# Kernel optimization log

Hardware: AMD Instinct MI355X
Metric: run time of the kernel (lower is better)

The kernel has to match this reference:

```python
import jax, jax.numpy as jnp
import numpy as np
import math

B, S, D, H = 2, 1024, 1024, 16
HD = D // H
MAX_ITERS = 4
BETA_0, BETA_DELTA = 0.8, 0.2
MOMENTUM = 0.2
FREQ_FACTOR, PHASE_OFFSET = 2.0, 0.0


def setup_inputs() -> dict:
    key = jax.random.key(0)
    ks = jax.random.split(key, 10)
    s = 1.0 / math.sqrt(D)
    return {
        "x": jax.random.normal(ks[0], (B, S, D), dtype=jnp.float32),
        "Wq": jax.random.normal(ks[1], (D, D), dtype=jnp.float32) * s,
        "bq": jnp.zeros((D,), dtype=jnp.float32),
        "Wk": jax.random.normal(ks[2], (D, D), dtype=jnp.float32) * s,
        "bk": jnp.zeros((D,), dtype=jnp.float32),
        "Wv": jax.random.normal(ks[3], (D, D), dtype=jnp.float32) * s,
        "bv": jnp.zeros((D,), dtype=jnp.float32),
        "Wo": jax.random.normal(ks[4], (D, D), dtype=jnp.float32) * s,
        "bo": jnp.zeros((D,), dtype=jnp.float32),
        "resonance_bias": jnp.zeros((1, H, 1, 1), dtype=jnp.float32),
        "phase_factors": jnp.full((1, H, 1, 1), 0.1, dtype=jnp.float32),
    }


def reference(x, Wq, bq, Wk, bk, Wv, bv, Wo, bo, resonance_bias, phase_factors):
    # Projections -> [B, H, S, HD]
    def split_heads(t):
        return t.reshape(B, S, H, HD).transpose(0, 2, 1, 3)

    q = split_heads(x @ Wq.T + bq)
    k = split_heads(x @ Wk.T + bk)
    v = split_heads(x @ Wv.T + bv)

    scale = 1.0 / math.sqrt(HD)
    attn = None
    for t in range(MAX_ITERS):
        # Phase modulation: shift Q/K by learned per-head phase factors
        t_norm = t / MAX_ITERS
        phase = jnp.sin(jnp.float32(FREQ_FACTOR * t_norm * math.pi + PHASE_OFFSET))
        q_mod = q + phase_factors * phase
        k_mod = k + phase_factors * phase
        # Temperature scheduling: inverse temperature grows each iteration
        beta = BETA_0 + BETA_DELTA * t
        scores = beta * scale * jnp.einsum("bhsd,bhtd->bhst", q_mod, k_mod) + resonance_bias
        attn_new = jax.nn.softmax(scores, axis=-1)
        # Momentum-based attention update
        attn = attn_new if attn is None else MOMENTUM * attn + (1.0 - MOMENTUM) * attn_new

    ctx = jnp.einsum("bhst,bhtd->bhsd", attn, v)  # [B,H,S,HD]
    ctx = ctx.transpose(0, 2, 1, 3).reshape(B, S, D)
    return ctx @ Wo.T + bo
```

## Files before the change

### kernel.cpp

```cpp
#include <hip/hip_runtime.h>
#include <hip/hip_bf16.h>
#include <math.h>

#define BB 2
#define SS 1024
#define DD 1024
#define HH 16
#define HD 64
#define BH (BB*HH)

typedef __attribute__((ext_vector_type(8))) short short8_t;
typedef __attribute__((ext_vector_type(4))) float f32x4;

#if __has_builtin(__builtin_amdgcn_exp2f)
#define EXP2(x) __builtin_amdgcn_exp2f(x)
#else
#define EXP2(x) exp2f(x)
#endif

__device__ __forceinline__ ushort f2bf(float f) {
    union { float f; unsigned u; } a; a.f = f;
    unsigned u = a.u;
    u += 0x7FFFu + ((u >> 16) & 1u);
    return (ushort)(u >> 16);
}
__device__ __forceinline__ float bf2f(ushort b) {
    union { unsigned u; float f; } a; a.u = ((unsigned)b) << 16;
    return a.f;
}
__device__ __forceinline__ unsigned pkbf(float a, float b) {
    unsigned r;
    asm("v_cvt_pk_bf16_f32 %0, %1, %2" : "=v"(r) : "v"(a), "v"(b));
    return r;
}

__global__ __launch_bounds__(256) void cvt_all_kernel(
    const float* __restrict__ x,  const float* __restrict__ wq,
    const float* __restrict__ wk, const float* __restrict__ wv,
    const float* __restrict__ wo,
    ushort* __restrict__ xb,  ushort* __restrict__ wqb, ushort* __restrict__ wkb,
    ushort* __restrict__ wvb, ushort* __restrict__ wob)
{
    int bid = blockIdx.x;
    const float* src; ushort* dst; int off;
    if (bid < 2048) { src = x; dst = xb; off = bid; }
    else {
        int seg = (bid - 2048) >> 10;
        off = (bid - 2048) & 1023;
        if (seg == 0)      { src = wq; dst = wqb; }
        else if (seg == 1) { src = wk; dst = wkb; }
        else if (seg == 2) { src = wv; dst = wvb; }
        else               { src = wo; dst = wob; }
    }
    int i = (off * 256 + threadIdx.x) * 4;
    float4 v = *reinterpret_cast<const float4*>(src + i);
    ushort4 o;
    o.x = f2bf(v.x); o.y = f2bf(v.y); o.z = f2bf(v.z); o.w = f2bf(v.w);
    *reinterpret_cast<ushort4*>(dst + i) = o;
}

template<int BM, int OUT_F32>
__device__ __forceinline__ void gemm_body(
    const ushort* __restrict__ A, const ushort* __restrict__ Bm,
    const float* __restrict__ bias, void* __restrict__ Cout,
    int N, int K, float scale)
{
    constexpr int BK = 32;
    __shared__ ushort lsa[BM * BK];
    __shared__ ushort lsb[128 * BK];
    const int tid  = threadIdx.x;
    const int lane = tid & 63;
    const int wave = tid >> 6;
    constexpr int RI = BM / 32;
    const int wrow = (wave >> 1) * (BM / 2);
    const int wcol = (wave & 1) * 64;
    const int tileM = blockIdx.y * BM;
    const int tileN = blockIdx.x * 128;
    const int fr  = lane & 15;
    const int fks = (lane >> 4) * 8;
    const int l4  = lane >> 2;
    const int lm4 = lane & 3;
    f32x4 acc[RI][4] = {};

    for (int kb = 0; kb < K; kb += BK) {
        __syncthreads();
        #pragma unroll
        for (int i = 0; i < BM / 64; ++i) {
            int chunk = wave * (BM / 64) + i;
            const ushort* g = A + (size_t)(tileM + chunk * 16 + l4) * K + kb + lm4 * 8;
            __builtin_amdgcn_global_load_lds(
                (const __attribute__((address_space(1))) unsigned*)g,
                (__attribute__((address_space(3))) unsigned*)&lsa[chunk * 512], 16, 0, 0);
        }
        #pragma unroll
        for (int i = 0; i < 2; ++i) {
            int chunk = wave * 2 + i;
            const ushort* g = Bm + (size_t)(tileN + chunk * 16 + l4) * K + kb + lm4 * 8;
            __builtin_amdgcn_global_load_lds(
                (const __attribute__((address_space(1))) unsigned*)g,
                (__attribute__((address_space(3))) unsigned*)&lsb[chunk * 512], 16, 0, 0);
        }
        __syncthreads();
        short8_t af[RI], bfg[4];
        #pragma unroll
        for (int r = 0; r < RI; ++r)
            af[r] = *reinterpret_cast<const short8_t*>(&lsa[(wrow + r * 16 + fr) * BK + fks]);
        #pragma unroll
        for (int c = 0; c < 4; ++c)
            bfg[c] = *reinterpret_cast<const short8_t*>(&lsb[(wcol + c * 16 + fr) * BK + fks]);
        #pragma unroll
        for (int r = 0; r < RI; ++r)
            #pragma unroll
            for (int c = 0; c < 4; ++c)
                acc[r][c] = __builtin_amdgcn_mfma_f32_16x16x32_bf16(af[r], bfg[c], acc[r][c], 0, 0, 0);
    }

    const int rr = (lane >> 4) * 4;
    #pragma unroll
    for (int r = 0; r < RI; ++r) {
        #pragma unroll
        for (int c = 0; c < 4; ++c) {
            int n = tileN + wcol + c * 16 + fr;
            float bv = bias[n];
            #pragma unroll
            for (int q = 0; q < 4; ++q) {
                int m = tileM + wrow + r * 16 + rr + q;
                float v = (acc[r][c][q] + bv) * scale;
                if (OUT_F32) ((float*)Cout)[(size_t)m * N + n] = v;
                else         ((ushort*)Cout)[(size_t)m * N + n] = f2bf(v);
            }
        }
    }
}

__global__ __launch_bounds__(256) void gemm_qkv_kernel(
    const ushort* __restrict__ xb,
    const ushort* __restrict__ wq, const ushort* __restrict__ wk, const ushort* __restrict__ wv,
    const float* __restrict__ bq, const float* __restrict__ bk, const float* __restrict__ bv,
    ushort* __restrict__ Qb, ushort* __restrict__ Kb, ushort* __restrict__ Vb, float qscale)
{
    const ushort* Bm; const float* bias; ushort* out; float sc;
    if (blockIdx.z == 0)      { Bm = wq; bias = bq; out = Qb; sc = qscale; }
    else if (blockIdx.z == 1) { Bm = wk; bias = bk; out = Kb; sc = 1.0f; }
    else                      { Bm = wv; bias = bv; out = Vb; sc = 1.0f; }
    gemm_body<128, 0>(xb, Bm, bias, out, DD, DD, sc);
}

__global__ __launch_bounds__(256) void gemm_out_kernel(
    const ushort* __restrict__ ctxb, const ushort* __restrict__ wo,
    const float* __restrict__ bo, float* __restrict__ out)
{
    gemm_body<64, 1>(ctxb, wo, bo, out, DD, DD, 1.0f);
}

__global__ __launch_bounds__(256) void tables_kernel(const ushort* __restrict__ Kb,
                                                     const float* __restrict__ pf,
                                                     float* __restrict__ E1, float* __restrict__ E3,
                                                     ushort* __restrict__ Kh,
                                                     float a1, float a3) {
    int idx = blockIdx.x * blockDim.x + threadIdx.x;
    int j  = idx & (SS - 1);
    int bh = idx >> 10;
    int b = bh >> 4, h = bh & 15;
    const ushort* kr = Kb + (size_t)(b * SS + j) * DD + h * HD;
    ushort* kout = Kh + (size_t)idx * HD;
    float s = 0.f;
    #pragma unroll
    for (int c = 0; c < HD; c += 8) {
        short8_t v = *reinterpret_cast<const short8_t*>(kr + c);
        *reinterpret_cast<short8_t*>(kout + c) = v;
        #pragma unroll
        for (int e = 0; e < 8; ++e) s += bf2f((ushort)v[e]);
    }
    float ph = pf[h];
    E1[idx] = __expf(a1 * ph * s);
    E3[idx] = __expf(a3 * ph * s);
}

__global__ __launch_bounds__(256) void transpose_v_kernel(const ushort* __restrict__ Vb,
                                                          ushort* __restrict__ Vt2) {
    __shared__ ushort t[64][72];
    int bh = blockIdx.x; int b = bh >> 4, h = bh & 15;
    int j0 = blockIdx.y * 64;
    #pragma unroll
    for (int s = 0; s < 2; ++s) {
        int ch = threadIdx.x + s * 256;
        int row = ch >> 3, c = (ch & 7) * 8;
        *reinterpret_cast<short8_t*>(&t[row][c]) =
            *reinterpret_cast<const short8_t*>(Vb + (size_t)(b * SS + j0 + row) * DD + h * HD + c);
    }
    __syncthreads();
    #pragma unroll
    for (int s = 0; s < 2; ++s) {
        int ch = threadIdx.x + s * 256;
        int drow = ch >> 3, c = (ch & 7) * 8;
        short8_t v;
        #pragma unroll
        for (int e = 0; e < 8; ++e) v[e] = (short)t[c + e][drow];
        int kb32 = (j0 + c) >> 5;
        int kk   = c & 31;
        *reinterpret_cast<short8_t*>(
            Vt2 + ((size_t)(bh * (SS / 32) + kb32) * HD + drow) * 32 + kk) = v;
    }
}

__global__ __launch_bounds__(256) void attn_kernel(
    const ushort* __restrict__ Qb, const ushort* __restrict__ Kh,
    const ushort* __restrict__ Vt2, const float* __restrict__ E1,
    const float* __restrict__ E3, ushort* __restrict__ ctxb)
{
    __shared__ ushort ycache[4][32][264];
    __shared__ float lbuf[4][4][32];
    const int wg  = blockIdx.x;
    const int swz = (wg & 7) * 128 + (wg >> 3);
    const int bh  = swz >> 5;
    const int qb  = (swz & 31) * 32;
    const int b = bh >> 4, h = bh & 15;
    const int wave = threadIdx.x >> 6;
    const int lane = threadIdx.x & 63;
    const int fr = lane & 15;
    const int g  = lane >> 4;
    const int fk = g * 8;

    const float wt[4] = {0.008f, 0.032f, 0.16f, 0.8f};

    const ushort* qbase0 = Qb + (size_t)(b * SS + qb + fr) * DD + h * HD;
    const ushort* qbase1 = Qb + (size_t)(b * SS + qb + 16 + fr) * DD + h * HD;
    const short8_t aq0a = *reinterpret_cast<const short8_t*>(qbase0 + fk);
    const short8_t aq1a = *reinterpret_cast<const short8_t*>(qbase0 + 32 + fk);
    const short8_t aq0b = *reinterpret_cast<const short8_t*>(qbase1 + fk);
    const short8_t aq1b = *reinterpret_cast<const short8_t*>(qbase1 + 32 + fk);

    const float* e1h = E1 + bh * SS;
    const float* e3h = E3 + bh * SS;
    const ushort* khead = Kh + (size_t)bh * SS * HD;
    const ushort* vhead = Vt2 + (size_t)bh * (SS / 32) * HD * 32;

    float lA[4][4] = {}, lB[4][4] = {};
    for (int it = 0; it < 4; ++it) {
        const int k0 = wave * 256 + it * 64;
        #pragma unroll
        for (int n = 0; n < 4; ++n) {
            const ushort* kb = khead + (size_t)(k0 + n * 16 + fr) * HD;
            short8_t bk0 = *reinterpret_cast<const short8_t*>(kb + fk);
            short8_t bk1 = *reinterpret_cast<const short8_t*>(kb + 32 + fk);
            f32x4 za = {0.f, 0.f, 0.f, 0.f};
            f32x4 zb = {0.f, 0.f, 0.f, 0.f};
            za = __builtin_amdgcn_mfma_f32_16x16x32_bf16(aq0a, bk0, za, 0, 0, 0);
            za = __builtin_amdgcn_mfma_f32_16x16x32_bf16(aq1a, bk1, za, 0, 0, 0);
            zb = __builtin_amdgcn_mfma_f32_16x16x32_bf16(aq0b, bk0, zb, 0, 0, 0);
            zb = __builtin_amdgcn_mfma_f32_16x16x32_bf16(aq1b, bk1, zb, 0, 0, 0);
            float e1v = e1h[k0 + n * 16 + fr];
            float e3v = e3h[k0 + n * 16 + fr];
            #pragma unroll
            for (int r = 0; r < 4; ++r) {
                float ya  = EXP2(za[r]);
                float ya2 = ya * ya;
                float ya4 = ya2 * ya2;
                float ya6 = ya4 * ya2;
                lA[0][r] += ya4;
                lA[1][r] += ya4 * ya * e1v;
                lA[2][r] += ya6;
                lA[3][r] += ya6 * ya * e3v;
                ycache[wave][g * 4 + r][it * 64 + n * 16 + fr] = f2bf(ya);
                float yb  = EXP2(zb[r]);
                float yb2 = yb * yb;
                float yb4 = yb2 * yb2;
                float yb6 = yb4 * yb2;
                lB[0][r] += yb4;
                lB[1][r] += yb4 * yb * e1v;
                lB[2][r] += yb6;
                lB[3][r] += yb6 * yb * e3v;
                ycache[wave][16 + g * 4 + r][it * 64 + n * 16 + fr] = f2bf(yb);
            }
        }
    }
    #pragma unroll
    for (int t = 0; t < 4; ++t)
        #pragma unroll
        for (int r = 0; r < 4; ++r) {
            float sa = lA[t][r];
            sa += __shfl_xor(sa, 1);
            sa += __shfl_xor(sa, 2);
            sa += __shfl_xor(sa, 4);
            sa += __shfl_xor(sa, 8);
            lA[t][r] = sa;
            float sb = lB[t][r];
            sb += __shfl_xor(sb, 1);
            sb += __shfl_xor(sb, 2);
            sb += __shfl_xor(sb, 4);
            sb += __shfl_xor(sb, 8);
            lB[t][r] = sb;
        }
    if (fr == 0) {
        #pragma unroll
        for (int t = 0; t < 4; ++t)
            #pragma unroll
            for (int r = 0; r < 4; ++r) {
                lbuf[wave][t][g * 4 + r]      = lA[t][r];
                lbuf[wave][t][16 + g * 4 + r] = lB[t][r];
            }
    }
    __syncthreads();

    float wlA[4], wlB[4];
    #pragma unroll
    for (int t = 0; t < 4; ++t) {
        float sa = lbuf[0][t][fr] + lbuf[1][t][fr] + lbuf[2][t][fr] + lbuf[3][t][fr];
        float sb = lbuf[0][t][16 + fr] + lbuf[1][t][16 + fr] + lbuf[2][t][16 + fr] + lbuf[3][t][16 + fr];
        wlA[t] = wt[t] / sa;
        wlB[t] = wt[t] / sb;
    }

    f32x4 caccA[4] = {}, caccB[4] = {};
    union FragU { short8_t s; unsigned u[4]; };
    for (int it = 0; it < 4; ++it) {
        const int k0 = wave * 256 + it * 64;
        #pragma unroll
        for (int half = 0; half < 2; ++half) {
            short8_t ya8 = *reinterpret_cast<const short8_t*>(
                &ycache[wave][fr][it * 64 + half * 32 + fk]);
            short8_t yb8 = *reinterpret_cast<const short8_t*>(
                &ycache[wave][16 + fr][it * 64 + half * 32 + fk]);
            const float* e1p = e1h + k0 + half * 32 + fk;
            const float* e3p = e3h + k0 + half * 32 + fk;
            float4 e1a = *reinterpret_cast<const float4*>(e1p);
            float4 e1b = *reinterpret_cast<const float4*>(e1p + 4);
            float4 e3a = *reinterpret_cast<const float4*>(e3p);
            float4 e3b = *reinterpret_cast<const float4*>(e3p + 4);
            FragU paA, paB;
            #pragma unroll
            for (int i = 0; i < 4; ++i) {
                float pva[2], pvb[2];
                #pragma unroll
                for (int j = 0; j < 2; ++j) {
                    const int e = 2 * i + j;
                    float e1v = (e < 4) ? ((const float*)&e1a)[e] : ((const float*)&e1b)[e - 4];
                    float e3v = (e < 4) ? ((const float*)&e3a)[e] : ((const float*)&e3b)[e - 4];
                    float ya  = bf2f((ushort)ya8[e]);
                    float ya2 = ya * ya;
                    float ya4 = ya2 * ya2;
                    float t1a = fmaf(ya, wlA[1] * e1v, wlA[0]);
                    float t2a = fmaf(ya, wlA[3] * e3v, wlA[2]);
                    pva[j] = ya4 * fmaf(ya2, t2a, t1a);
                    float yb  = bf2f((ushort)yb8[e]);
                    float yb2 = yb * yb;
                    float yb4 = yb2 * yb2;
                    float t1b = fmaf(yb, wlB[1] * e1v, wlB[0]);
                    float t2b = fmaf(yb, wlB[3] * e3v, wlB[2]);
                    pvb[j] = yb4 * fmaf(yb2, t2b, t1b);
                }
                paA.u[i] = pkbf(pva[0], pva[1]);
                paB.u[i] = pkbf(pvb[0], pvb[1]);
            }
            const ushort* vt = vhead + (size_t)((k0 + half * 32) >> 5) * HD * 32;
            #pragma unroll
            for (int n2 = 0; n2 < 4; ++n2) {
                short8_t v = *reinterpret_cast<const short8_t*>(
                    vt + (n2 * 16 + fr) * 32 + fk);
                caccA[n2] = __builtin_amdgcn_mfma_f32_16x16x32_bf16(paA.s, v, caccA[n2], 0, 0, 0);
                caccB[n2] = __builtin_amdgcn_mfma_f32_16x16x32_bf16(paB.s, v, caccB[n2], 0, 0, 0);
            }
        }
    }

    __syncthreads();
    float* ctxp = (float*)&ycache[wave][0][0];
    #pragma unroll
    for (int n2 = 0; n2 < 4; ++n2)
        #pragma unroll
        for (int q = 0; q < 4; ++q) {
            ctxp[(g * 4 + q) * 68 + n2 * 16 + fr]        = caccA[n2][q];
            ctxp[(16 + g * 4 + q) * 68 + n2 * 16 + fr]   = caccB[n2][q];
        }
    __syncthreads();

    const int d0 = (threadIdx.x & 15) * 4;
    float* base = (float*)&ycache[0][0][0];
    #pragma unroll
    for (int rr = 0; rr < 2; ++rr) {
        int row = rr * 16 + (threadIdx.x >> 4);
        float4 s0 = *reinterpret_cast<float4*>(base + 0 * 4224 + row * 68 + d0);
        float4 s1 = *reinterpret_cast<float4*>(base + 1 * 4224 + row * 68 + d0);
        float4 s2 = *reinterpret_cast<float4*>(base + 2 * 4224 + row * 68 + d0);
        float4 s3 = *reinterpret_cast<float4*>(base + 3 * 4224 + row * 68 + d0);
        float ox = s0.x + s1.x + s2.x + s3.x;
        float oy = s0.y + s1.y + s2.y + s3.y;
        float oz = s0.z + s1.z + s2.z + s3.z;
        float ow = s0.w + s1.w + s2.w + s3.w;
        uint2 o;
        o.x = pkbf(ox, oy);
        o.y = pkbf(oz, ow);
        size_t off = (size_t)(b * SS + qb + row) * DD + h * HD + d0;
        *reinterpret_cast<uint2*>(ctxb + off) = o;
    }
}

extern "C" void kernel_launch(void* const* d_in, const int* in_sizes, int n_in,
                              void* d_out, int out_size, void* d_ws, size_t ws_size,
                              hipStream_t stream) {
    const float* x  = (const float*)d_in[0];
    const float* Wq = (const float*)d_in[1];
    const float* bq = (const float*)d_in[2];
    const float* Wk = (const float*)d_in[3];
    const float* bk = (const float*)d_in[4];
    const float* Wv = (const float*)d_in[5];
    const float* bv = (const float*)d_in[6];
    const float* Wo = (const float*)d_in[7];
    const float* bo = (const float*)d_in[8];
    const float* pf = (const float*)d_in[10];

    ushort* xb   = (ushort*)d_ws;
    ushort* wqb  = xb  + (size_t)2 * 1024 * 1024;
    ushort* wkb  = wqb + (size_t)1024 * 1024;
    ushort* wvb  = wkb + (size_t)1024 * 1024;
    ushort* wob  = wvb + (size_t)1024 * 1024;
    ushort* Qb   = wob + (size_t)1024 * 1024;
    ushort* Kb   = Qb  + (size_t)2 * 1024 * 1024;
    ushort* Vb   = Kb  + (size_t)2 * 1024 * 1024;
    ushort* Vt2  = Vb  + (size_t)2 * 1024 * 1024;
    ushort* ctxb = Vt2 + (size_t)2 * 1024 * 1024;
    float*  E1p  = (float*)(ctxb + (size_t)2 * 1024 * 1024);
    float*  E3p  = E1p + (size_t)BH * SS;
    ushort* Kh   = xb;

    float ph[4], ctv[4];
    for (int t = 0; t < 4; ++t) {
        double tn = (double)t / 4.0;
        ph[t]  = sinf((float)(2.0 * tn * M_PI + 0.0));
        ctv[t] = (float)((0.8 + 0.2 * (double)t) * 0.125);
    }
    const double LOG2E = 1.44269504088896340736;
    float qscale = (float)(0.025 * LOG2E);
    float a1 = ctv[1] * ph[1];
    float a3 = ctv[3] * ph[3];

    cvt_all_kernel<<<6144, 256, 0, stream>>>(x, Wq, Wk, Wv, Wo, xb, wqb, wkb, wvb, wob);

    gemm_qkv_kernel<<<dim3(8, 16, 3), 256, 0, stream>>>(xb, wqb, wkb, wvb, bq, bk, bv,
                                                        Qb, Kb, Vb, qscale);

    tables_kernel<<<BH * SS / 256, 256, 0, stream>>>(Kb, pf, E1p, E3p, Kh, a1, a3);
    transpose_v_kernel<<<dim3(BH, SS / 64), 256, 0, stream>>>(Vb, Vt2);

    attn_kernel<<<1024, 256, 0, stream>>>(Qb, Kh, Vt2, E1p, E3p, ctxb);

    gemm_out_kernel<<<dim3(8, 32), 256, 0, stream>>>(ctxb, wob, bo, (float*)d_out);
}
```

Measured before the change: 109.2 us.

## Write K and V in attention layouts from QKV GEMM epilogue, drop transpose kernel

The QKV GEMM epilogue now writes K directly in head-major [bh][j][d] layout and V directly in the blocked transposed layout the attention kernel consumes. This removes the separate V transpose kernel and the K copy inside the tables kernel. The QKV GEMM tile height also drops from 128 to 64, doubling the grid. The scattered 2-byte epilogue stores for V (stride 32 along d) are less coalesced, and smaller tiles reduce operand reuse.

```diff
diff --git a/kernel.cpp b/kernel.cpp
--- a/kernel.cpp
+++ b/kernel.cpp
@@ -63,7 +63,7 @@
 __device__ __forceinline__ void gemm_body(
     const ushort* __restrict__ A, const ushort* __restrict__ Bm,
     const float* __restrict__ bias, void* __restrict__ Cout,
-    int N, int K, float scale)
+    int N, int K, float scale, int omode)
 {
     constexpr int BK = 32;
     __shared__ ushort lsa[BM * BK];
@@ -126,8 +126,19 @@
             for (int q = 0; q < 4; ++q) {
                 int m = tileM + wrow + r * 16 + rr + q;
                 float v = (acc[r][c][q] + bv) * scale;
-                if (OUT_F32) ((float*)Cout)[(size_t)m * N + n] = v;
-                else         ((ushort*)Cout)[(size_t)m * N + n] = f2bf(v);
+                if (OUT_F32) {
+                    ((float*)Cout)[(size_t)m * N + n] = v;
+                } else if (omode == 0) {
+                    ((ushort*)Cout)[(size_t)m * N + n] = f2bf(v);
+                } else {
+                    int bh = ((m >> 10) << 4) + (n >> 6);
+                    int j  = m & 1023;
+                    int d  = n & 63;
+                    if (omode == 2)
+                        ((ushort*)Cout)[((size_t)bh * 1024 + j) * 64 + d] = f2bf(v);
+                    else
+                        ((ushort*)Cout)[(((size_t)(bh * 32 + (j >> 5)) * 64 + d)) * 32 + (j & 31)] = f2bf(v);
+                }
             }
         }
     }
@@ -137,71 +148,40 @@
     const ushort* __restrict__ xb,
     const ushort* __restrict__ wq, const ushort* __restrict__ wk, const ushort* __restrict__ wv,
     const float* __restrict__ bq, const float* __restrict__ bk, const float* __restrict__ bv,
-    ushort* __restrict__ Qb, ushort* __restrict__ Kb, ushort* __restrict__ Vb, float qscale)
+    ushort* __restrict__ Qb, ushort* __restrict__ Kh, ushort* __restrict__ Vt2, float qscale)
 {
-    const ushort* Bm; const float* bias; ushort* out; float sc;
-    if (blockIdx.z == 0)      { Bm = wq; bias = bq; out = Qb; sc = qscale; }
-    else if (blockIdx.z == 1) { Bm = wk; bias = bk; out = Kb; sc = 1.0f; }
-    else                      { Bm = wv; bias = bv; out = Vb; sc = 1.0f; }
-    gemm_body<128, 0>(xb, Bm, bias, out, DD, DD, sc);
+    const ushort* Bm; const float* bias; ushort* out; float sc; int omode;
+    if (blockIdx.z == 0)      { Bm = wq; bias = bq; out = Qb;  sc = qscale; omode = 0; }
+    else if (blockIdx.z == 1) { Bm = wk; bias = bk; out = Kh;  sc = 1.0f;   omode = 2; }
+    else                      { Bm = wv; bias = bv; out = Vt2; sc = 1.0f;   omode = 3; }
+    gemm_body<64, 0>(xb, Bm, bias, out, DD, DD, sc, omode);
 }
 
 __global__ __launch_bounds__(256) void gemm_out_kernel(
     const ushort* __restrict__ ctxb, const ushort* __restrict__ wo,
     const float* __restrict__ bo, float* __restrict__ out)
 {
-    gemm_body<64, 1>(ctxb, wo, bo, out, DD, DD, 1.0f);
-}
-
-__global__ __launch_bounds__(256) void tables_kernel(const ushort* __restrict__ Kb,
+    gemm_body<64, 1>(ctxb, wo, bo, out, DD, DD, 1.0f, 0);
+}
+
+__global__ __launch_bounds__(256) void tables_kernel(const ushort* __restrict__ Kh,
                                                      const float* __restrict__ pf,
                                                      float* __restrict__ E1, float* __restrict__ E3,
-                                                     ushort* __restrict__ Kh,
                                                      float a1, float a3) {
     int idx = blockIdx.x * blockDim.x + threadIdx.x;
-    int j  = idx & (SS - 1);
     int bh = idx >> 10;
-    int b = bh >> 4, h = bh & 15;
-    const ushort* kr = Kb + (size_t)(b * SS + j) * DD + h * HD;
-    ushort* kout = Kh + (size_t)idx * HD;
+    int h = bh & 15;
+    const ushort* kr = Kh + (size_t)idx * HD;
     float s = 0.f;
     #pragma unroll
     for (int c = 0; c < HD; c += 8) {
         short8_t v = *reinterpret_cast<const short8_t*>(kr + c);
-        *reinterpret_cast<short8_t*>(kout + c) = v;
         #pragma unroll
         for (int e = 0; e < 8; ++e) s += bf2f((ushort)v[e]);
     }
     float ph = pf[h];
     E1[idx] = __expf(a1 * ph * s);
     E3[idx] = __expf(a3 * ph * s);
-}
-
-__global__ __launch_bounds__(256) void transpose_v_kernel(const ushort* __restrict__ Vb,
-                                                          ushort* __restrict__ Vt2) {
-    __shared__ ushort t[64][72];
-    int bh = blockIdx.x; int b = bh >> 4, h = bh & 15;
-    int j0 = blockIdx.y * 64;
-    #pragma unroll
-    for (int s = 0; s < 2; ++s) {
-        int ch = threadIdx.x + s * 256;
-        int row = ch >> 3, c = (ch & 7) * 8;
-        *reinterpret_cast<short8_t*>(&t[row][c]) =
-            *reinterpret_cast<const short8_t*>(Vb + (size_t)(b * SS + j0 + row) * DD + h * HD + c);
-    }
-    __syncthreads();
-    #pragma unroll
-    for (int s = 0; s < 2; ++s) {
-        int ch = threadIdx.x + s * 256;
-        int drow = ch >> 3, c = (ch & 7) * 8;
-        short8_t v;
-        #pragma unroll
-        for (int e = 0; e < 8; ++e) v[e] = (short)t[c + e][drow];
-        int kb32 = (j0 + c) >> 5;
-        int kk   = c & 31;
-        *reinterpret_cast<short8_t*>(
-            Vt2 + ((size_t)(bh * (SS / 32) + kb32) * HD + drow) * 32 + kk) = v;
-    }
 }
 
 __global__ __launch_bounds__(256) void attn_kernel(
@@ -416,13 +396,11 @@
     ushort* wvb  = wkb + (size_t)1024 * 1024;
     ushort* wob  = wvb + (size_t)1024 * 1024;
     ushort* Qb   = wob + (size_t)1024 * 1024;
-    ushort* Kb   = Qb  + (size_t)2 * 1024 * 1024;
-    ushort* Vb   = Kb  + (size_t)2 * 1024 * 1024;
-    ushort* Vt2  = Vb  + (size_t)2 * 1024 * 1024;
+    ushort* Kh   = Qb  + (size_t)2 * 1024 * 1024;
+    ushort* Vt2  = Kh  + (size_t)2 * 1024 * 1024;
     ushort* ctxb = Vt2 + (size_t)2 * 1024 * 1024;
     float*  E1p  = (float*)(ctxb + (size_t)2 * 1024 * 1024);
     float*  E3p  = E1p + (size_t)BH * SS;
-    ushort* Kh   = xb;
 
     float ph[4], ctv[4];
     for (int t = 0; t < 4; ++t) {
@@ -437,11 +415,10 @@
 
     cvt_all_kernel<<<6144, 256, 0, stream>>>(x, Wq, Wk, Wv, Wo, xb, wqb, wkb, wvb, wob);
 
-    gemm_qkv_kernel<<<dim3(8, 16, 3), 256, 0, stream>>>(xb, wqb, wkb, wvb, bq, bk, bv,
-                                                        Qb, Kb, Vb, qscale);
-
-    tables_kernel<<<BH * SS / 256, 256, 0, stream>>>(Kb, pf, E1p, E3p, Kh, a1, a3);
-    transpose_v_kernel<<<dim3(BH, SS / 64), 256, 0, stream>>>(Vb, Vt2);
+    gemm_qkv_kernel<<<dim3(8, 32, 3), 256, 0, stream>>>(xb, wqb, wkb, wvb, bq, bk, bv,
+                                                        Qb, Kh, Vt2, qscale);
+
+    tables_kernel<<<BH * SS / 256, 256, 0, stream>>>(Kh, pf, E1p, E3p, a1, a3);
 
     attn_kernel<<<1024, 256, 0, stream>>>(Qb, Kh, Vt2, E1p, E3p, ctxb);
 
```

Measured after the change: 105.0 us. 1.04x faster.
